# Optimization experiments

Hardware: AMD Instinct MI355X
Metric: run time of the kernel (lower is better)

The kernel has to match this reference:

```python
import jax, jax.numpy as jnp
import numpy as np

WINDOW = 60
DEPTH = 3
HIDDEN = 256
LN_EPS = 1e-5


def _lyndon_indices(d):
    # Lyndon words over alphabet {0..d-1}, lengths 2 and 3, lexicographic order
    # (signatory mode='words' extracts expanded-logsig coefficients at Lyndon words).
    i2 = np.array([(i, j) for i in range(d) for j in range(d) if (i, j) < (j, i)], dtype=np.int32)
    i3 = np.array([(i, j, k) for i in range(d) for j in range(d) for k in range(d)
                   if (i, j, k) < (j, k, i) and (i, j, k) < (k, i, j)], dtype=np.int32)
    return i2, i3


def _logsig_features(x):
    # x: [b, s, c] -> logsignature of time-augmented sliding windows: [b*s, sig_channels]
    b, s, c = x.shape
    d = c + 1
    # replicate-padded sliding windows via clipped gather (matches F.pad replicate + unfold)
    pos = jnp.clip(jnp.arange(s)[:, None] + jnp.arange(WINDOW)[None, :] - (WINDOW - 1), 0, s - 1)
    windows = x[:, pos, :]                                   # [b, s, W, c]
    t = jnp.linspace(0.0, 1.0, WINDOW, dtype=x.dtype)        # time augmentation channel
    t_b = jnp.broadcast_to(t[None, None, :, None], (b, s, WINDOW, 1))
    aug = jnp.concatenate([t_b, windows], axis=-1).reshape(b * s, WINDOW, d)
    N = b * s
    # basepoint=True: prepend zero point -> increments include the first point itself
    inc = jnp.diff(aug, axis=1, prepend=jnp.zeros((N, 1, d), aug.dtype))  # [N, W, d]
    inc_t = jnp.transpose(inc, (1, 0, 2))                    # [W, N, d]

    def chen_step(carry, v):
        S1, S2, S3 = carry
        vv = jnp.einsum('ni,nj->nij', v, v)
        vvv = jnp.einsum('nij,nk->nijk', vv, v)
        nS3 = S3 + jnp.einsum('nij,nk->nijk', S2, v) \
                 + 0.5 * jnp.einsum('ni,njk->nijk', S1, vv) + vvv / 6.0
        nS2 = S2 + jnp.einsum('ni,nj->nij', S1, v) + 0.5 * vv
        nS1 = S1 + v
        return (nS1, nS2, nS3), None

    init = (jnp.zeros((N, d), x.dtype), jnp.zeros((N, d, d), x.dtype), jnp.zeros((N, d, d, d), x.dtype))
    (S1, S2, S3), _ = jax.lax.scan(chen_step, init, inc_t)
    # log in truncated tensor algebra: log(1+x) = x - x^2/2 + x^3/3
    L1 = S1
    L2 = S2 - 0.5 * jnp.einsum('ni,nj->nij', S1, S1)
    L3 = (S3 - 0.5 * (jnp.einsum('ni,njk->nijk', S1, S2) + jnp.einsum('nij,nk->nijk', S2, S1))
          + jnp.einsum('ni,nj,nk->nijk', S1, S1, S1) / 3.0)
    i2, i3 = _lyndon_indices(d)
    f2 = L2[:, i2[:, 0], i2[:, 1]]
    f3 = L3[:, i3[:, 0], i3[:, 1], i3[:, 2]]
    return jnp.concatenate([L1, f2, f3], axis=-1)            # [N, sig_channels]


def setup_inputs() -> dict:
    key = jax.random.key(0)
    ks = jax.random.split(key, 5)
    b, s, c = 8, 2048, 8
    d = c + 1
    sig_channels = d + (d * d - d) // 2 + (d ** 3 - d) // 3  # 285 for d=9
    h2 = 2 * HIDDEN
    x = jax.random.normal(ks[0], (b, s, c), dtype=jnp.float32)
    w1 = jax.random.normal(ks[1], (sig_channels, h2), dtype=jnp.float32) / np.sqrt(sig_channels)
    b1 = jnp.zeros((h2,), jnp.float32)
    ln_g = jnp.ones((h2,), jnp.float32)
    ln_b = jnp.zeros((h2,), jnp.float32)
    w2 = jax.random.normal(ks[2], (h2, HIDDEN), dtype=jnp.float32) / np.sqrt(h2)
    b2 = jnp.zeros((HIDDEN,), jnp.float32)
    return {"x": x, "w1": w1, "b1": b1, "ln_g": ln_g, "ln_b": ln_b, "w2": w2, "b2": b2}


def reference(x, w1, b1, ln_g, ln_b, w2, b2):
    b, s, _ = x.shape
    feats = _logsig_features(x)                              # [b*s, sig_channels]
    h = jax.nn.gelu(feats @ w1 + b1, approximate=False)      # torch default GELU (erf)
    mu = jnp.mean(h, axis=-1, keepdims=True)
    var = jnp.var(h, axis=-1, keepdims=True)
    h = (h - mu) / jnp.sqrt(var + LN_EPS) * ln_g + ln_b      # LayerNorm; Dropout is eval no-op
    out = h @ w2 + b2
    return out.reshape(b, s, -1)
```

## Files before the change

kernel.cpp:

```cpp
#include <hip/hip_runtime.h>
#include <hip/hip_bf16.h>
#include <cstdint>
#include <cstddef>

typedef short short8 __attribute__((ext_vector_type(8)));
typedef float f32x4 __attribute__((ext_vector_type(4)));
typedef float f32x2 __attribute__((ext_vector_type(2)));

#define NS    2048
#define KPAD  288
#define H2    512
#define HID   256
#define WPB   7
#define SBLK  293
#define KLDS1 296
#define KLDS2 520

#define MFMA(a,b,c) __builtin_amdgcn_mfma_f32_16x16x32_bf16((a),(b),(c),0,0,0)

__device__ __forceinline__ float geluf(float x) {
    return 0.5f * x * (1.0f + erff(x * 0.70710678118654752f));
}
__device__ __forceinline__ f32x4 shfl4(f32x4 v, int d) {
    f32x4 r;
    r[0] = __shfl_xor(v[0], d); r[1] = __shfl_xor(v[1], d);
    r[2] = __shfl_xor(v[2], d); r[3] = __shfl_xor(v[3], d);
    return r;
}

struct Tbl3 { short col[729]; };
static constexpr Tbl3 make_tbl3() {
    Tbl3 t{};
    for (int x = 0; x < 729; ++x) t.col[x] = -1;
    int r = 0;
    for (int i = 0; i < 9; ++i)
        for (int j = 0; j < 9; ++j)
            for (int k = 0; k < 9; ++k) {
                bool lt1 = (i < j) || (i == j && (j < k || (j == k && k < i)));
                bool lt2 = (i < k) || (i == k && (j < i || (j == i && k < j)));
                if (lt1 && lt2) { t.col[(i*9+j)*9+k] = (short)(45 + r); ++r; }
            }
    return t;
}
static constexpr Tbl3 TBL3 = make_tbl3();

#define SIG_STEP(VA_,VB_,VC_) { \
    const float hh = 0.5f * S1i + vi * (1.0f/6.0f); \
    const float ra = S2ra + hh * (VA_); \
    const float rb = S2rb + hh * (VB_); \
    const float rc = S2rc + hh * (VC_); \
    const f32x2 ra2 = {ra, ra}, rb2 = {rb, rb}, rc2 = {rc, rc}; \
    S3sa += ra * v0; S3pa0 += ra2*vp0; S3pa1 += ra2*vp1; S3pa2 += ra2*vp2; S3pa3 += ra2*vp3; \
    S3sb += rb * v0; S3pb0 += rb2*vp0; S3pb1 += rb2*vp1; S3pb2 += rb2*vp2; S3pb3 += rb2*vp3; \
    S3sc += rc * v0; S3pc0 += rc2*vp0; S3pc1 += rc2*vp1; S3pc2 += rc2*vp2; S3pc3 += rc2*vp3; \
    const float aa = S1i + 0.5f * vi; \
    S2ra += aa * (VA_); S2rb += aa * (VB_); S2rc += aa * (VC_); \
    S1i += vi; }

#define SIG_MAIN(VA_,VB_,VC_) { \
    { const float* xr = &X[(g0 - lo) * 8]; \
      const float4 e0 = *(const float4*)xr; \
      const float4 e1 = *(const float4*)(xr + 4); \
      const float rs = xr[ioff]; \
      const float v0 = 0.0f; \
      const f32x2 vp0 = {e0.x, e0.y}, vp1 = {e0.z, e0.w}, vp2 = {e1.x, e1.y}, vp3 = {e1.z, e1.w}; \
      const float vi = (ci == 0) ? 0.0f : rs; \
      SIG_STEP(VA_,VB_,VC_) } \
    const float* pd = &PD[(sm59 + 1 - lo + 59) * 8]; \
    float4 d0 = *(const float4*)pd; \
    float4 d1 = *(const float4*)(pd + 4); \
    float rn = pd[ioff]; \
    _Pragma("unroll 4") \
    for (int j = 1; j < 60; ++j) { \
      const float4 e0 = d0; const float4 e1 = d1; const float rs = rn; \
      pd += 8; \
      d0 = *(const float4*)pd; d1 = *(const float4*)(pd + 4); rn = pd[ioff]; \
      const float v0 = DT; \
      const f32x2 vp0 = {e0.x, e0.y}, vp1 = {e0.z, e0.w}, vp2 = {e1.x, e1.y}, vp3 = {e1.z, e1.w}; \
      const float vi = (ci == 0) ? DT : rs; \
      SIG_STEP(VA_,VB_,VC_) \
    } }

#define SIG_ST(RA,RB,RC) \
    if (act) { \
        if ((RA) == 0) S1buf[widx * 9 + ci] = S1i; \
        float* sb = &S2buf[widx * 81 + ci * 9]; \
        sb[RA] = S2ra; sb[RB] = S2rb; sb[RC] = S2rc; \
    }

#define S3EL0(SL) S3s##SL
#define S3EL1(SL) S3p##SL##0[0]
#define S3EL2(SL) S3p##SL##0[1]
#define S3EL3(SL) S3p##SL##1[0]
#define S3EL4(SL) S3p##SL##1[1]
#define S3EL5(SL) S3p##SL##2[0]
#define S3EL6(SL) S3p##SL##2[1]
#define S3EL7(SL) S3p##SL##3[0]
#define S3EL8(SL) S3p##SL##3[1]

#define SIG_E2(SL,J2) if (ci < (J2)) { \
    const float val2 = S2r##SL - 0.5f * S1i * s1v##J2; \
    const int col2 = 9 + ci*8 - (ci*(ci-1))/2 + ((J2) - ci - 1); \
    frow[col2] = __float2bfloat16(val2); }

#define SIG_E3(SL,R,K) { const int col3 = TBL3.col[tb + (R)*9 + (K)]; \
    if (col3 >= 0) { \
        const float val3 = S3EL##K(SL) \
            - 0.5f * (S1i * S2w[(R)*9+(K)] + S2r##SL * s1v##K) \
            + S1i * s1v##R * s1v##K * (1.0f/3.0f); \
        frow[col3] = __float2bfloat16(val3); } }

#define SIG_E3R(SL,R) SIG_E3(SL,R,0) SIG_E3(SL,R,1) SIG_E3(SL,R,2) SIG_E3(SL,R,3) \
    SIG_E3(SL,R,4) SIG_E3(SL,R,5) SIG_E3(SL,R,6) SIG_E3(SL,R,7) SIG_E3(SL,R,8)

#define SIG_EMIT(RA,RB,RC) \
    if (act) { \
        if ((RA) == 0) { \
            frow[ci] = __float2bfloat16(S1i); \
            if (ci == 0) { \
                const __hip_bfloat16 z16 = __float2bfloat16(0.0f); \
                frow[285] = z16; frow[286] = z16; frow[287] = z16; \
            } \
        } \
        SIG_E2(a,RA) SIG_E2(b,RB) SIG_E2(c,RC) \
        SIG_E3R(a,RA) SIG_E3R(b,RB) SIG_E3R(c,RC) \
    }

__global__ __launch_bounds__(192) __attribute__((amdgpu_waves_per_eu(1, 6)))
void sig_kernel(const float* __restrict__ x, __hip_bfloat16* __restrict__ feats) {
    __shared__ __align__(16) float X[66 * 8];
    __shared__ __align__(16) float PD[126 * 8];
    __shared__ float S2buf[WPB * 81];
    __shared__ float S1buf[WPB * 9];

    const int blk = blockIdx.x;
    const int b   = blk / SBLK;
    const int s0  = (blk % SBLK) * WPB;
    const int lo  = (s0 - 59 > 0) ? (s0 - 59) : 0;
    const int hi  = (s0 + WPB - 1 < NS - 1) ? (s0 + WPB - 1) : (NS - 1);
    const int nrow = hi - lo + 1;
    const int tid = threadIdx.x;

    {
        const float4* src = (const float4*)(x + ((size_t)b * NS + lo) * 8);
        float4* X4 = (float4*)X;
        const int n4 = nrow * 2;
        for (int t = tid; t < n4; t += 192) X4[t] = src[t];
    }
    __syncthreads();
    {
        const float4* X4 = (const float4*)X;
        float4* PD4 = (float4*)PD;
        for (int t = tid; t < 252; t += 192) {
            const int p = t >> 1;
            const int r = p - 59;
            float4 dv = {0.f, 0.f, 0.f, 0.f};
            if (r > 0 && r < nrow) {
                const float4 a = X4[t - 118], bb = X4[t - 120];
                dv.x = a.x - bb.x; dv.y = a.y - bb.y; dv.z = a.z - bb.z; dv.w = a.w - bb.w;
            }
            PD4[t] = dv;
        }
    }
    __syncthreads();

    const int t3    = tid >> 6;
    const int lt    = tid & 63;
    const int widx0 = lt / 9;
    const int ci    = lt - widx0 * 9;
    const bool act  = (lt < 63) && (s0 + widx0 < NS);
    const int widx  = (widx0 < WPB - 1) ? widx0 : WPB - 1;
    int s = s0 + widx; if (s > NS - 1) s = NS - 1;

    float S3sa=0.f, S3sb=0.f, S3sc=0.f;
    f32x2 S3pa0={0.f,0.f},S3pa1={0.f,0.f},S3pa2={0.f,0.f},S3pa3={0.f,0.f};
    f32x2 S3pb0={0.f,0.f},S3pb1={0.f,0.f},S3pb2={0.f,0.f},S3pb3={0.f,0.f};
    f32x2 S3pc0={0.f,0.f},S3pc1={0.f,0.f},S3pc2={0.f,0.f},S3pc3={0.f,0.f};
    float S2ra=0.f, S2rb=0.f, S2rc=0.f;
    float S1i = 0.f;
    const int ioff = (ci > 0) ? (ci - 1) : 0;
    const int sm59 = s - 59;
    const int g0   = (sm59 > 0) ? sm59 : 0;
    const float DT = 1.0f / 59.0f;

    if (t3 == 0)      { SIG_MAIN(v0,   e0.x, e0.y) }
    else if (t3 == 1) { SIG_MAIN(e0.z, e0.w, e1.x) }
    else              { SIG_MAIN(e1.y, e1.z, e1.w) }

    if (t3 == 0)      { SIG_ST(0,1,2) }
    else if (t3 == 1) { SIG_ST(3,4,5) }
    else              { SIG_ST(6,7,8) }
    __syncthreads();

    const float* s1p = &S1buf[widx * 9];
    const float s1v0=s1p[0], s1v1=s1p[1], s1v2=s1p[2], s1v3=s1p[3], s1v4=s1p[4];
    const float s1v5=s1p[5], s1v6=s1p[6], s1v7=s1p[7], s1v8=s1p[8];
    const float* S2w = &S2buf[widx * 81];
    const int tb = ci * 81;
    __hip_bfloat16* frow = feats + (size_t)(b * NS + s) * KPAD;

    if (t3 == 0)      { SIG_EMIT(0,1,2) }
    else if (t3 == 1) { SIG_EMIT(3,4,5) }
    else              { SIG_EMIT(6,7,8) }
}

__global__ __launch_bounds__(512) void convert_weights(
        const float* __restrict__ w1, const float* __restrict__ w2,
        const float* __restrict__ lng, const float* __restrict__ lnb,
        const float* __restrict__ b2,
        __hip_bfloat16* __restrict__ w1T, __hip_bfloat16* __restrict__ w2g,
        float* __restrict__ gw, float* __restrict__ cvec) {
    const int blk = blockIdx.x;
    const int k = threadIdx.x;
    if (blk < 512) {
        if (k < KPAD) {
            const float v = (k < 285) ? w1[(size_t)k * H2 + blk] : 0.0f;
            w1T[(size_t)blk * KPAD + k] = __float2bfloat16(v);
        }
        return;
    }
    const int n = blk - 512;
    const float wv = w2[(size_t)k * HID + n];
    const float a = lng[k] * wv;
    const float c = lnb[k] * wv;
    w2g[(size_t)n * H2 + k] = __float2bfloat16(a);
    float ra = a, rc = c;
#pragma unroll
    for (int d = 1; d < 64; d <<= 1) { ra += __shfl_xor(ra, d); rc += __shfl_xor(rc, d); }
    __shared__ float r1[8], r2[8];
    const int wv_ = k >> 6, ln = k & 63;
    if (ln == 0) { r1[wv_] = ra; r2[wv_] = rc; }
    __syncthreads();
    if (k == 0) {
        float sa = 0.f, sc = 0.f;
#pragma unroll
        for (int i = 0; i < 8; ++i) { sa += r1[i]; sc += r2[i]; }
        gw[n] = sa; cvec[n] = sc + b2[n];
    }
}

__global__ __launch_bounds__(256) __attribute__((amdgpu_waves_per_eu(1, 4)))
void gemm1_kernel(const __hip_bfloat16* __restrict__ feats,
                  const __hip_bfloat16* __restrict__ w1T,
                  const float* __restrict__ b1,
                  __hip_bfloat16* __restrict__ h1,
                  float* __restrict__ stats) {
    __shared__ __align__(16) __hip_bfloat16 ldsB[64 * KLDS1];
    const int tid  = threadIdx.x;
    const int wave = tid >> 6;
    const int lane = tid & 63;
    const int quad = lane >> 4;
    const int l16  = lane & 15;
    const int m0   = blockIdx.x * 128 + wave * 32;
    const int n0   = blockIdx.y * 64;
    const int nb   = blockIdx.y;

    for (int c = tid; c < 64 * 36; c += 256) {
        const int n = c / 36, k8 = c - n * 36;
        *(short8*)(ldsB + n * KLDS1 + k8 * 8) =
            *(const short8*)(w1T + (size_t)(n0 + n) * KPAD + k8 * 8);
    }
    __syncthreads();

    const __hip_bfloat16* a0 = feats + (size_t)(m0 + l16) * KPAD + quad * 8;
    const __hip_bfloat16* a1 = feats + (size_t)(m0 + 16 + l16) * KPAD + quad * 8;
    const __hip_bfloat16* bb = ldsB + l16 * KLDS1 + quad * 8;

    f32x4 acc00={0,0,0,0},acc01={0,0,0,0},acc02={0,0,0,0},acc03={0,0,0,0};
    f32x4 acc10={0,0,0,0},acc11={0,0,0,0},acc12={0,0,0,0},acc13={0,0,0,0};
#pragma unroll
    for (int kt = 0; kt < 9; ++kt) {
        const int ko = kt * 32;
        const short8 av0 = *(const short8*)(a0 + ko);
        const short8 av1 = *(const short8*)(a1 + ko);
        const short8 bv0 = *(const short8*)(bb + ko);
        const short8 bv1 = *(const short8*)(bb + 16 * KLDS1 + ko);
        const short8 bv2 = *(const short8*)(bb + 32 * KLDS1 + ko);
        const short8 bv3 = *(const short8*)(bb + 48 * KLDS1 + ko);
        acc00 = MFMA(av0, bv0, acc00); acc01 = MFMA(av0, bv1, acc01);
        acc02 = MFMA(av0, bv2, acc02); acc03 = MFMA(av0, bv3, acc03);
        acc10 = MFMA(av1, bv0, acc10); acc11 = MFMA(av1, bv1, acc11);
        acc12 = MFMA(av1, bv2, acc12); acc13 = MFMA(av1, bv3, acc13);
    }

    const float bias0 = b1[n0 +  0 + l16];
    const float bias1 = b1[n0 + 16 + l16];
    const float bias2 = b1[n0 + 32 + l16];
    const float bias3 = b1[n0 + 48 + l16];
#define G1G(A,B) { A[0]=geluf(A[0]+B); A[1]=geluf(A[1]+B); A[2]=geluf(A[2]+B); A[3]=geluf(A[3]+B); }
    G1G(acc00,bias0) G1G(acc01,bias1) G1G(acc02,bias2) G1G(acc03,bias3)
    G1G(acc10,bias0) G1G(acc11,bias1) G1G(acc12,bias2) G1G(acc13,bias3)
#undef G1G

    f32x4 s0 = acc00 + acc01 + acc02 + acc03;
    f32x4 q0 = acc00*acc00 + acc01*acc01 + acc02*acc02 + acc03*acc03;
    f32x4 s1 = acc10 + acc11 + acc12 + acc13;
    f32x4 q1 = acc10*acc10 + acc11*acc11 + acc12*acc12 + acc13*acc13;
    s0 += shfl4(s0,1); q0 += shfl4(q0,1); s1 += shfl4(s1,1); q1 += shfl4(q1,1);
    s0 += shfl4(s0,2); q0 += shfl4(q0,2); s1 += shfl4(s1,2); q1 += shfl4(q1,2);
    s0 += shfl4(s0,4); q0 += shfl4(q0,4); s1 += shfl4(s1,4); q1 += shfl4(q1,4);
    s0 += shfl4(s0,8); q0 += shfl4(q0,8); s1 += shfl4(s1,8); q1 += shfl4(q1,8);
    if (l16 == 0) {
#pragma unroll
        for (int r = 0; r < 4; ++r) {
            const int r0 = m0 + quad * 4 + r;
            stats[r0 * 16 + nb] = s0[r]; stats[r0 * 16 + 8 + nb] = q0[r];
            const int r1 = r0 + 16;
            stats[r1 * 16 + nb] = s1[r]; stats[r1 * 16 + 8 + nb] = q1[r];
        }
    }

    {
        __hip_bfloat16* hp = h1 + (size_t)(m0 + quad * 4) * H2;
        const int c0 = n0 + l16;
#pragma unroll
        for (int r = 0; r < 4; ++r) {
            hp[(size_t)r * H2 + c0     ] = __float2bfloat16(acc00[r]);
            hp[(size_t)r * H2 + c0 + 16] = __float2bfloat16(acc01[r]);
            hp[(size_t)r * H2 + c0 + 32] = __float2bfloat16(acc02[r]);
            hp[(size_t)r * H2 + c0 + 48] = __float2bfloat16(acc03[r]);
        }
        __hip_bfloat16* hp2 = hp + (size_t)16 * H2;
#pragma unroll
        for (int r = 0; r < 4; ++r) {
            hp2[(size_t)r * H2 + c0     ] = __float2bfloat16(acc10[r]);
            hp2[(size_t)r * H2 + c0 + 16] = __float2bfloat16(acc11[r]);
            hp2[(size_t)r * H2 + c0 + 32] = __float2bfloat16(acc12[r]);
            hp2[(size_t)r * H2 + c0 + 48] = __float2bfloat16(acc13[r]);
        }
    }
}

__global__ __launch_bounds__(256) __attribute__((amdgpu_waves_per_eu(1, 4)))
void gemm2_kernel(const __hip_bfloat16* __restrict__ h1,
                  const __hip_bfloat16* __restrict__ w2g,
                  const float* __restrict__ stats,
                  const float* __restrict__ gw,
                  const float* __restrict__ cvec,
                  float* __restrict__ out) {
    __shared__ __align__(16) __hip_bfloat16 ldsB[32 * KLDS2];
    const int tid  = threadIdx.x;
    const int wave = tid >> 6;
    const int lane = tid & 63;
    const int quad = lane >> 4;
    const int l16  = lane & 15;
    const int m0   = blockIdx.x * 128 + wave * 32;
    const int n0   = blockIdx.y * 32;

    for (int c = tid; c < 32 * 64; c += 256) {
        const int n = c >> 6, k8 = c & 63;
        *(short8*)(ldsB + n * KLDS2 + k8 * 8) =
            *(const short8*)(w2g + (size_t)(n0 + n) * H2 + k8 * 8);
    }
    __syncthreads();

    const __hip_bfloat16* a0 = h1 + (size_t)(m0 + l16) * H2 + quad * 8;
    const __hip_bfloat16* a1 = h1 + (size_t)(m0 + 16 + l16) * H2 + quad * 8;
    const __hip_bfloat16* bb = ldsB + l16 * KLDS2 + quad * 8;

    f32x4 acc00={0,0,0,0},acc01={0,0,0,0},acc10={0,0,0,0},acc11={0,0,0,0};
#pragma unroll
    for (int kt = 0; kt < 16; ++kt) {
        const int ko = kt * 32;
        const short8 av0 = *(const short8*)(a0 + ko);
        const short8 av1 = *(const short8*)(a1 + ko);
        const short8 bv0 = *(const short8*)(bb + ko);
        const short8 bv1 = *(const short8*)(bb + 16 * KLDS2 + ko);
        acc00 = MFMA(av0, bv0, acc00); acc01 = MFMA(av0, bv1, acc01);
        acc10 = MFMA(av1, bv0, acc10); acc11 = MFMA(av1, bv1, acc11);
    }

    const int c0 = n0 + l16, c1 = c0 + 16;
    const float gw0 = gw[c0], gw1 = gw[c1];
    const float cv0 = cvec[c0], cv1 = cvec[c1];
#define G2EP(mf) { \
    const int rbase = m0 + (mf)*16 + quad*4; \
    _Pragma("unroll") \
    for (int r = 0; r < 4; ++r) { \
        const int row = rbase + r; \
        const float4 sA = *(const float4*)&stats[row*16]; \
        const float4 sB = *(const float4*)&stats[row*16+4]; \
        const float4 qA = *(const float4*)&stats[row*16+8]; \
        const float4 qB = *(const float4*)&stats[row*16+12]; \
        const float su = sA.x+sA.y+sA.z+sA.w + sB.x+sB.y+sB.z+sB.w; \
        const float qu = qA.x+qA.y+qA.z+qA.w + qB.x+qB.y+qB.z+qB.w; \
        const float mu = su * (1.0f/512.0f); \
        const float rsv = rsqrtf(qu*(1.0f/512.0f) - mu*mu + 1e-5f); \
        out[(size_t)row*HID + c0] = rsv*(acc##mf##0[r] - mu*gw0) + cv0; \
        out[(size_t)row*HID + c1] = rsv*(acc##mf##1[r] - mu*gw1) + cv1; \
    } }
    G2EP(0) G2EP(1)
#undef G2EP
}

extern "C" void kernel_launch(void* const* d_in, const int* in_sizes, int n_in,
                              void* d_out, int out_size, void* d_ws, size_t ws_size,
                              hipStream_t stream) {
    const float* x   = (const float*)d_in[0];
    const float* w1  = (const float*)d_in[1];
    const float* b1  = (const float*)d_in[2];
    const float* lng = (const float*)d_in[3];
    const float* lnb = (const float*)d_in[4];
    const float* w2  = (const float*)d_in[5];
    const float* b2  = (const float*)d_in[6];
    float* out = (float*)d_out;

    char* ws = (char*)d_ws;
    __hip_bfloat16* feats = (__hip_bfloat16*)(ws);
    __hip_bfloat16* h1    = (__hip_bfloat16*)(ws + 9437184);
    __hip_bfloat16* w1T   = (__hip_bfloat16*)(ws + 26214400);
    __hip_bfloat16* w2g   = (__hip_bfloat16*)(ws + 26509312);
    float*          gw    = (float*)(ws + 26771456);
    float*          cvec  = (float*)(ws + 26775552);
    float*          stats = (float*)(ws + 26779648);

    convert_weights<<<dim3(768), dim3(512), 0, stream>>>(w1, w2, lng, lnb, b2,
                                                         w1T, w2g, gw, cvec);
    sig_kernel<<<dim3(8 * SBLK), dim3(192), 0, stream>>>(x, feats);
    gemm1_kernel<<<dim3(128, 8), dim3(256), 0, stream>>>(feats, w1T, b1, h1, stats);
    gemm2_kernel<<<dim3(128, 8), dim3(256), 0, stream>>>(h1, w2g, stats, gw, cvec, out);
}
```

Before: 164.8 us.

## Stage A tiles in LDS and shrink GEMM block tiles to 64 rows

Both GEMM kernels now load the activation tile (feats or h1) into shared memory alongside the weight tile, and read MFMA operands from LDS instead of global memory. Block M-tiles shrink from 128 to 64 rows and the grid doubles, so per-wave work drops. In gemm1 the four waves now form a 2x2 split over M and N, which doubles the LayerNorm partial-stat slots per row from 8 to 16. The aim is more blocks for occupancy and coalesced staged loads. The cost is more total weight-tile reloads across blocks and higher LDS use per block.

```diff
diff --git a/kernel.cpp b/kernel.cpp
--- a/kernel.cpp
+++ b/kernel.cpp
@@ -239,114 +239,110 @@
     }
 }
 
-__global__ __launch_bounds__(256) __attribute__((amdgpu_waves_per_eu(1, 4)))
+__global__ __launch_bounds__(256)
 void gemm1_kernel(const __hip_bfloat16* __restrict__ feats,
                   const __hip_bfloat16* __restrict__ w1T,
                   const float* __restrict__ b1,
                   __hip_bfloat16* __restrict__ h1,
                   float* __restrict__ stats) {
+    __shared__ __align__(16) __hip_bfloat16 ldsA[64 * KLDS1];
     __shared__ __align__(16) __hip_bfloat16 ldsB[64 * KLDS1];
     const int tid  = threadIdx.x;
     const int wave = tid >> 6;
     const int lane = tid & 63;
     const int quad = lane >> 4;
     const int l16  = lane & 15;
-    const int m0   = blockIdx.x * 128 + wave * 32;
+    const int m0   = blockIdx.x * 64;
     const int n0   = blockIdx.y * 64;
-    const int nb   = blockIdx.y;
 
     for (int c = tid; c < 64 * 36; c += 256) {
         const int n = c / 36, k8 = c - n * 36;
+        *(short8*)(ldsA + n * KLDS1 + k8 * 8) =
+            *(const short8*)(feats + (size_t)(m0 + n) * KPAD + k8 * 8);
         *(short8*)(ldsB + n * KLDS1 + k8 * 8) =
             *(const short8*)(w1T + (size_t)(n0 + n) * KPAD + k8 * 8);
     }
     __syncthreads();
 
-    const __hip_bfloat16* a0 = feats + (size_t)(m0 + l16) * KPAD + quad * 8;
-    const __hip_bfloat16* a1 = feats + (size_t)(m0 + 16 + l16) * KPAD + quad * 8;
-    const __hip_bfloat16* bb = ldsB + l16 * KLDS1 + quad * 8;
-
-    f32x4 acc00={0,0,0,0},acc01={0,0,0,0},acc02={0,0,0,0},acc03={0,0,0,0};
-    f32x4 acc10={0,0,0,0},acc11={0,0,0,0},acc12={0,0,0,0},acc13={0,0,0,0};
+    const int mh = (wave >> 1) * 32;
+    const int nh = (wave & 1) * 32;
+    const __hip_bfloat16* ab = ldsA + (mh + l16) * KLDS1 + quad * 8;
+    const __hip_bfloat16* bb = ldsB + (nh + l16) * KLDS1 + quad * 8;
+
+    f32x4 acc00={0,0,0,0},acc01={0,0,0,0},acc10={0,0,0,0},acc11={0,0,0,0};
 #pragma unroll
     for (int kt = 0; kt < 9; ++kt) {
         const int ko = kt * 32;
-        const short8 av0 = *(const short8*)(a0 + ko);
-        const short8 av1 = *(const short8*)(a1 + ko);
+        const short8 av0 = *(const short8*)(ab + ko);
+        const short8 av1 = *(const short8*)(ab + 16 * KLDS1 + ko);
         const short8 bv0 = *(const short8*)(bb + ko);
         const short8 bv1 = *(const short8*)(bb + 16 * KLDS1 + ko);
-        const short8 bv2 = *(const short8*)(bb + 32 * KLDS1 + ko);
-        const short8 bv3 = *(const short8*)(bb + 48 * KLDS1 + ko);
         acc00 = MFMA(av0, bv0, acc00); acc01 = MFMA(av0, bv1, acc01);
-        acc02 = MFMA(av0, bv2, acc02); acc03 = MFMA(av0, bv3, acc03);
         acc10 = MFMA(av1, bv0, acc10); acc11 = MFMA(av1, bv1, acc11);
-        acc12 = MFMA(av1, bv2, acc12); acc13 = MFMA(av1, bv3, acc13);
-    }
-
-    const float bias0 = b1[n0 +  0 + l16];
-    const float bias1 = b1[n0 + 16 + l16];
-    const float bias2 = b1[n0 + 32 + l16];
-    const float bias3 = b1[n0 + 48 + l16];
+    }
+
+    const float bias0 = b1[n0 + nh + l16];
+    const float bias1 = b1[n0 + nh + 16 + l16];
 #define G1G(A,B) { A[0]=geluf(A[0]+B); A[1]=geluf(A[1]+B); A[2]=geluf(A[2]+B); A[3]=geluf(A[3]+B); }
-    G1G(acc00,bias0) G1G(acc01,bias1) G1G(acc02,bias2) G1G(acc03,bias3)
-    G1G(acc10,bias0) G1G(acc11,bias1) G1G(acc12,bias2) G1G(acc13,bias3)
+    G1G(acc00,bias0) G1G(acc01,bias1) G1G(acc10,bias0) G1G(acc11,bias1)
 #undef G1G
 
-    f32x4 s0 = acc00 + acc01 + acc02 + acc03;
-    f32x4 q0 = acc00*acc00 + acc01*acc01 + acc02*acc02 + acc03*acc03;
-    f32x4 s1 = acc10 + acc11 + acc12 + acc13;
-    f32x4 q1 = acc10*acc10 + acc11*acc11 + acc12*acc12 + acc13*acc13;
+    f32x4 s0 = acc00 + acc01, q0 = acc00*acc00 + acc01*acc01;
+    f32x4 s1 = acc10 + acc11, q1 = acc10*acc10 + acc11*acc11;
     s0 += shfl4(s0,1); q0 += shfl4(q0,1); s1 += shfl4(s1,1); q1 += shfl4(q1,1);
     s0 += shfl4(s0,2); q0 += shfl4(q0,2); s1 += shfl4(s1,2); q1 += shfl4(q1,2);
     s0 += shfl4(s0,4); q0 += shfl4(q0,4); s1 += shfl4(s1,4); q1 += shfl4(q1,4);
     s0 += shfl4(s0,8); q0 += shfl4(q0,8); s1 += shfl4(s1,8); q1 += shfl4(q1,8);
+    const int nb2 = blockIdx.y * 2 + (wave & 1);
     if (l16 == 0) {
 #pragma unroll
         for (int r = 0; r < 4; ++r) {
-            const int r0 = m0 + quad * 4 + r;
-            stats[r0 * 16 + nb] = s0[r]; stats[r0 * 16 + 8 + nb] = q0[r];
+            const int r0 = m0 + mh + quad * 4 + r;
+            stats[r0 * 32 + nb2] = s0[r]; stats[r0 * 32 + 16 + nb2] = q0[r];
             const int r1 = r0 + 16;
-            stats[r1 * 16 + nb] = s1[r]; stats[r1 * 16 + 8 + nb] = q1[r];
+            stats[r1 * 32 + nb2] = s1[r]; stats[r1 * 32 + 16 + nb2] = q1[r];
         }
     }
 
     {
-        __hip_bfloat16* hp = h1 + (size_t)(m0 + quad * 4) * H2;
-        const int c0 = n0 + l16;
+        __hip_bfloat16* hp = h1 + (size_t)(m0 + mh + quad * 4) * H2;
+        const int c0 = n0 + nh + l16;
 #pragma unroll
         for (int r = 0; r < 4; ++r) {
             hp[(size_t)r * H2 + c0     ] = __float2bfloat16(acc00[r]);
             hp[(size_t)r * H2 + c0 + 16] = __float2bfloat16(acc01[r]);
-            hp[(size_t)r * H2 + c0 + 32] = __float2bfloat16(acc02[r]);
-            hp[(size_t)r * H2 + c0 + 48] = __float2bfloat16(acc03[r]);
         }
         __hip_bfloat16* hp2 = hp + (size_t)16 * H2;
 #pragma unroll
         for (int r = 0; r < 4; ++r) {
             hp2[(size_t)r * H2 + c0     ] = __float2bfloat16(acc10[r]);
             hp2[(size_t)r * H2 + c0 + 16] = __float2bfloat16(acc11[r]);
-            hp2[(size_t)r * H2 + c0 + 32] = __float2bfloat16(acc12[r]);
-            hp2[(size_t)r * H2 + c0 + 48] = __float2bfloat16(acc13[r]);
-        }
-    }
-}
-
-__global__ __launch_bounds__(256) __attribute__((amdgpu_waves_per_eu(1, 4)))
+        }
+    }
+}
+
+__global__ __launch_bounds__(256)
 void gemm2_kernel(const __hip_bfloat16* __restrict__ h1,
                   const __hip_bfloat16* __restrict__ w2g,
                   const float* __restrict__ stats,
                   const float* __restrict__ gw,
                   const float* __restrict__ cvec,
                   float* __restrict__ out) {
+    __shared__ __align__(16) __hip_bfloat16 ldsA[64 * KLDS2];
     __shared__ __align__(16) __hip_bfloat16 ldsB[32 * KLDS2];
     const int tid  = threadIdx.x;
     const int wave = tid >> 6;
     const int lane = tid & 63;
     const int quad = lane >> 4;
     const int l16  = lane & 15;
-    const int m0   = blockIdx.x * 128 + wave * 32;
+    const int m0   = blockIdx.x * 64;
     const int n0   = blockIdx.y * 32;
 
+    for (int c = tid; c < 64 * 64; c += 256) {
+        const int n = c >> 6, k8 = c & 63;
+        *(short8*)(ldsA + n * KLDS2 + k8 * 8) =
+            *(const short8*)(h1 + (size_t)(m0 + n) * H2 + k8 * 8);
+    }
     for (int c = tid; c < 32 * 64; c += 256) {
         const int n = c >> 6, k8 = c & 63;
         *(short8*)(ldsB + n * KLDS2 + k8 * 8) =
@@ -354,43 +350,42 @@
     }
     __syncthreads();
 
-    const __hip_bfloat16* a0 = h1 + (size_t)(m0 + l16) * H2 + quad * 8;
-    const __hip_bfloat16* a1 = h1 + (size_t)(m0 + 16 + l16) * H2 + quad * 8;
+    const int mh = wave * 16;
+    const __hip_bfloat16* ab = ldsA + (mh + l16) * KLDS2 + quad * 8;
     const __hip_bfloat16* bb = ldsB + l16 * KLDS2 + quad * 8;
 
-    f32x4 acc00={0,0,0,0},acc01={0,0,0,0},acc10={0,0,0,0},acc11={0,0,0,0};
+    f32x4 acc0={0,0,0,0}, acc1={0,0,0,0};
 #pragma unroll
     for (int kt = 0; kt < 16; ++kt) {
         const int ko = kt * 32;
-        const short8 av0 = *(const short8*)(a0 + ko);
-        const short8 av1 = *(const short8*)(a1 + ko);
+        const short8 av  = *(const short8*)(ab + ko);
         const short8 bv0 = *(const short8*)(bb + ko);
         const short8 bv1 = *(const short8*)(bb + 16 * KLDS2 + ko);
-        acc00 = MFMA(av0, bv0, acc00); acc01 = MFMA(av0, bv1, acc01);
-        acc10 = MFMA(av1, bv0, acc10); acc11 = MFMA(av1, bv1, acc11);
+        acc0 = MFMA(av, bv0, acc0);
+        acc1 = MFMA(av, bv1, acc1);
     }
 
     const int c0 = n0 + l16, c1 = c0 + 16;
     const float gw0 = gw[c0], gw1 = gw[c1];
     const float cv0 = cvec[c0], cv1 = cvec[c1];
-#define G2EP(mf) { \
-    const int rbase = m0 + (mf)*16 + quad*4; \
-    _Pragma("unroll") \
-    for (int r = 0; r < 4; ++r) { \
-        const int row = rbase + r; \
-        const float4 sA = *(const float4*)&stats[row*16]; \
-        const float4 sB = *(const float4*)&stats[row*16+4]; \
-        const float4 qA = *(const float4*)&stats[row*16+8]; \
-        const float4 qB = *(const float4*)&stats[row*16+12]; \
-        const float su = sA.x+sA.y+sA.z+sA.w + sB.x+sB.y+sB.z+sB.w; \
-        const float qu = qA.x+qA.y+qA.z+qA.w + qB.x+qB.y+qB.z+qB.w; \
-        const float mu = su * (1.0f/512.0f); \
-        const float rsv = rsqrtf(qu*(1.0f/512.0f) - mu*mu + 1e-5f); \
-        out[(size_t)row*HID + c0] = rsv*(acc##mf##0[r] - mu*gw0) + cv0; \
-        out[(size_t)row*HID + c1] = rsv*(acc##mf##1[r] - mu*gw1) + cv1; \
-    } }
-    G2EP(0) G2EP(1)
-#undef G2EP
+    const int rbase = m0 + mh + quad * 4;
+#pragma unroll
+    for (int r = 0; r < 4; ++r) {
+        const int row = rbase + r;
+        const float* sp = &stats[row * 32];
+        float su = 0.f, qu = 0.f;
+#pragma unroll
+        for (int i = 0; i < 4; ++i) {
+            const float4 sv = *(const float4*)(sp + i * 4);
+            const float4 qv = *(const float4*)(sp + 16 + i * 4);
+            su += sv.x + sv.y + sv.z + sv.w;
+            qu += qv.x + qv.y + qv.z + qv.w;
+        }
+        const float mu  = su * (1.0f / 512.0f);
+        const float rsv = rsqrtf(qu * (1.0f / 512.0f) - mu * mu + 1e-5f);
+        out[(size_t)row * HID + c0] = rsv * (acc0[r] - mu * gw0) + cv0;
+        out[(size_t)row * HID + c1] = rsv * (acc1[r] - mu * gw1) + cv1;
+    }
 }
 
 extern "C" void kernel_launch(void* const* d_in, const int* in_sizes, int n_in,
@@ -417,6 +412,6 @@
     convert_weights<<<dim3(768), dim3(512), 0, stream>>>(w1, w2, lng, lnb, b2,
                                                          w1T, w2g, gw, cvec);
     sig_kernel<<<dim3(8 * SBLK), dim3(192), 0, stream>>>(x, feats);
-    gemm1_kernel<<<dim3(128, 8), dim3(256), 0, stream>>>(feats, w1T, b1, h1, stats);
-    gemm2_kernel<<<dim3(128, 8), dim3(256), 0, stream>>>(h1, w2g, stats, gw, cvec, out);
-}
+    gemm1_kernel<<<dim3(256, 8), dim3(256), 0, stream>>>(feats, w1T, b1, h1, stats);
+    gemm2_kernel<<<dim3(256, 8), dim3(256), 0, stream>>>(h1, w2g, stats, gw, cvec, out);
+}
```

Result: slower. 193.3 us (+17.3%).
